# Performance work log

Measured on AMD Instinct MI355X. Metric: run time of the kernel, lower is better.

The kernel has to match this reference:

```python
import jax, jax.numpy as jnp
import numpy as np

B = 16384          # batch_size
NF = 50            # n_fields
K = 16             # embedding_dim
V = 1_000_000      # input_dim (vocab)
H = 400            # fc hidden
NNZ = B * NF


def _xavier(key, shape):
    fan_in, fan_out = shape
    lim = (6.0 / (fan_in + fan_out)) ** 0.5
    return jax.random.uniform(key, shape, minval=-lim, maxval=lim, dtype=jnp.float32)


def setup_inputs() -> dict:
    key = jax.random.key(0)
    ks = jax.random.split(key, 12)
    feats = jax.random.randint(ks[0], (NNZ,), 0, V)
    # n_fields contiguous features per sample (required by view(batch_size,-1))
    index = jnp.repeat(jnp.arange(B), NF)
    values = jax.random.uniform(ks[1], (NNZ,), dtype=jnp.float32)
    bias = jnp.zeros((1, 1), jnp.float32)
    weights = _xavier(ks[2], (V, 1))
    embedding = _xavier(ks[3], (V, K))
    d = NF * K  # 800
    W0 = _xavier(ks[4], (d, H))
    b0 = jax.random.normal(ks[5], (1, 1), jnp.float32)
    W1 = _xavier(ks[6], (H, H))
    b1 = jax.random.normal(ks[7], (1, 1), jnp.float32)
    W2 = _xavier(ks[8], (H, 1))
    b2 = jax.random.normal(ks[9], (1, 1), jnp.float32)
    return dict(index=index, feats=feats, values=values, bias=bias,
                weights=weights, embedding=embedding,
                W0=W0, b0=b0, W1=W1, b1=b1, W2=W2, b2=b2, batch_size=B)


def reference(index, feats, values, bias, weights, embedding,
              W0, b0, W1, b1, W2, b2, batch_size):
    # gather (F.embedding)
    w = weights[feats, 0]              # [nnz]
    emb = embedding[feats]             # [nnz, K]

    # first order: segment-sum of w*v, plus bias ([B] + [1,1] -> [1,B], as in torch)
    first = jax.ops.segment_sum(w * values, index, num_segments=batch_size) + bias

    # second order: FM pooling trick, fused over all K dims in one segment reduce
    ev = emb * values[:, None]                                        # [nnz, K]
    s1 = jax.ops.segment_sum(ev, index, num_segments=batch_size)      # [B, K]
    s2 = jax.ops.segment_sum(ev * ev, index, num_segments=batch_size) # [B, K]
    second = 0.5 * jnp.sum(s1 * s1 - s2, axis=1)                      # [B]

    # higher order MLP (relu on every layer, scalar biases)
    x = emb.reshape(batch_size, -1)    # [B, NF*K]
    x = jax.nn.relu(x @ W0 + b0)
    x = jax.nn.relu(x @ W1 + b1)
    x = jax.nn.relu(x @ W2 + b2)       # [B, 1]
    higher = x.reshape(-1)             # [B]

    return jax.nn.sigmoid(first + second + higher)  # [1, B]
```

## Files before the change

kernel.cpp:

```cpp
#include <hip/hip_runtime.h>
#include <hip/hip_bf16.h>


#define BATCH 16384
#define NFLD  50
#define EK    16
#define DDIM  800
#define HDIM  400
#define HPAD  416
#define NPAD  512

#define TB_W0 400
#define TB_W1 208
#define TBLK  (TB_W0 + TB_W1)
#define GBLK  (BATCH / 16)

#define MROWS 64
#define NCOLS 448
#define WCOLS 112
#define NFRAG 7
#define P1    (DDIM / 32)
#define P2    (HPAD / 32)
#define H0S   424
#define SBUF  16384
#define SBUF2 14336

#define VMCNT(N) asm volatile("s_waitcnt vmcnt(" #N ")" ::: "memory")

typedef __attribute__((ext_vector_type(8))) __bf16 bf16x8;
typedef __attribute__((ext_vector_type(4))) float  f32x4;

typedef const __attribute__((address_space(1))) unsigned int* gas_u32p;
typedef __attribute__((address_space(3))) unsigned int*       las_u32p;

__device__ __forceinline__ void gld_lds16(const void* g, void* l) {
    __builtin_amdgcn_global_load_lds((gas_u32p)g, (las_u32p)l, 16, 0, 0);
}

__device__ __forceinline__ void bar() {
    __builtin_amdgcn_sched_barrier(0);
    __builtin_amdgcn_s_barrier();
    __builtin_amdgcn_sched_barrier(0);
}

__global__ __launch_bounds__(256) void prep_kernel(
    const float* __restrict__ W0, const float* __restrict__ W1,
    __hip_bfloat16* __restrict__ W0t, __hip_bfloat16* __restrict__ W1t,
    const int* __restrict__ feats, const float* __restrict__ values,
    const float* __restrict__ biasp, const float* __restrict__ weights,
    const float* __restrict__ embedding,
    float* __restrict__ fs, __hip_bfloat16* __restrict__ x)
{
    const int bid = blockIdx.x;
    if (bid < TBLK) {
        const int which = bid >= TB_W0;
        const int i  = which ? bid - TB_W0 : bid;
        const int nx = which ? 13 : 25;
        const int bx = i % nx, by = i / nx;
        const float* src = which ? W1 : W0;
        __hip_bfloat16* dst = which ? W1t : W0t;
        const int srcK = which ? HDIM : DDIM;
        const int dstCols = which ? HPAD : DDIM;

        __shared__ float tile[32][33];
        const int tx = threadIdx.x & 31, ty = threadIdx.x >> 5;
        const int k0 = bx * 32, n0 = by * 32;
#pragma unroll
        for (int r = 0; r < 4; ++r) {
            int k = k0 + ty + r * 8;
            int n = n0 + tx;
            float v = (k < srcK && n < HDIM) ? src[(long)k * HDIM + n] : 0.f;
            tile[ty + r * 8][tx] = v;
        }
        __syncthreads();
#pragma unroll
        for (int r = 0; r < 4; ++r) {
            int n = n0 + ty + r * 8;
            int k = k0 + tx;
            if (k < dstCols)
                dst[(long)n * dstCols + k] = __float2bfloat16(tile[tx][ty + r * 8]);
        }
        return;
    }

    const int wave = threadIdx.x >> 6;
    const int lane = threadIdx.x & 63;
    const int r    = lane >> 2, c = lane & 3;
    const int sbase = (bid - TBLK) * 16 + wave * 4;

    int   f[4] = {0, 0, 0, 0};
    float v[4] = {0.f, 0.f, 0.f, 0.f};
    float wsum[4] = {0.f, 0.f, 0.f, 0.f};
#pragma unroll
    for (int q = 0; q < 4; ++q) {
        const long base = (long)(sbase + q) * NFLD;
        if (lane < NFLD) {
            f[q] = feats[base + lane];
            v[q] = values[base + lane];
            wsum[q] = weights[f[q]] * v[q];
        }
    }

    int   fj[4][4]; float vj[4][4];
#pragma unroll
    for (int q = 0; q < 4; ++q)
#pragma unroll
        for (int p = 0; p < 4; ++p) {
            const int j = p * 16 + r;
            if (p < 3 || r < 2) {
                fj[q][p] = __shfl(f[q], j);
                vj[q][p] = __shfl(v[q], j);
            }
        }
    float4 e[4][4];
#pragma unroll
    for (int q = 0; q < 4; ++q)
#pragma unroll
        for (int p = 0; p < 4; ++p)
            if (p < 3 || r < 2)
                e[q][p] = *(const float4*)(embedding + (long)fj[q][p] * EK + c * 4);

#pragma unroll
    for (int q = 0; q < 4; ++q) {
        const int s = sbase + q;
        f32x4 s1 = {0.f, 0.f, 0.f, 0.f}, s2 = {0.f, 0.f, 0.f, 0.f};
#pragma unroll
        for (int p = 0; p < 4; ++p) {
            const int j = p * 16 + r;
            if (p < 3 || r < 2) {
                f32x4 ef = {e[q][p].x, e[q][p].y, e[q][p].z, e[q][p].w};
                f32x4 ev = ef * vj[q][p];
                s1 += ev;
                s2 += ev * ev;
                __hip_bfloat16 pk[4] = {
                    __float2bfloat16(e[q][p].x), __float2bfloat16(e[q][p].y),
                    __float2bfloat16(e[q][p].z), __float2bfloat16(e[q][p].w)};
                *(uint2*)&x[(long)s * DDIM + j * EK + c * 4] = *(uint2*)pk;
            }
        }
#pragma unroll
        for (int m = 4; m <= 32; m <<= 1) {
            s1.x += __shfl_xor(s1.x, m); s1.y += __shfl_xor(s1.y, m);
            s1.z += __shfl_xor(s1.z, m); s1.w += __shfl_xor(s1.w, m);
            s2.x += __shfl_xor(s2.x, m); s2.y += __shfl_xor(s2.y, m);
            s2.z += __shfl_xor(s2.z, m); s2.w += __shfl_xor(s2.w, m);
        }
        float t = (s1.x * s1.x - s2.x) + (s1.y * s1.y - s2.y)
                + (s1.z * s1.z - s2.z) + (s1.w * s1.w - s2.w);
        t += __shfl_xor(t, 1); t += __shfl_xor(t, 2);
        float w = wsum[q];
        w += __shfl_xor(w, 1);  w += __shfl_xor(w, 2);
        w += __shfl_xor(w, 4);  w += __shfl_xor(w, 8);
        w += __shfl_xor(w, 16); w += __shfl_xor(w, 32);
        if (lane == 0) fs[s] = w + 0.5f * t + biasp[0];
    }
}

__global__ __launch_bounds__(512, 2) void fused_mlp_kernel(
    const __hip_bfloat16* __restrict__ x,
    const __hip_bfloat16* __restrict__ W0t, const __hip_bfloat16* __restrict__ W1t,
    const float* __restrict__ b0p, const float* __restrict__ b1p,
    const float* __restrict__ W2, const float* __restrict__ b2p,
    const float* __restrict__ fs, float* __restrict__ out)
{
    __shared__ __align__(16) __hip_bfloat16 sS[3 * SBUF];
    __shared__ __align__(16) __hip_bfloat16 h0p[MROWS * H0S];
    __shared__ float red[MROWS][4];

    const int tid  = threadIdx.x;
    const int wave = tid >> 6, lane = tid & 63;
    const int l16  = lane & 15, quad = lane >> 4;
    const int waveM = wave & 1, waveN = wave >> 1;
    const int m0 = blockIdx.x * MROWS;

    const int rl  = lane >> 2;
    const int swc = ((lane & 3) ^ ((lane >> 3) & 3)) * 8;
    const int qsw = (quad ^ ((l16 >> 1) & 3)) * 8;

    const float b0 = b0p[0];
    const float b1 = b1p[0];

    auto stage1 = [&](int p, int b) {
        const int k0 = p * 32;
        __hip_bfloat16* dst = sS + b * SBUF;
#pragma unroll
        for (int c = 0; c < 4; ++c) {
            const int idx = wave * 4 + c;
            const __hip_bfloat16* src = (idx < 4)
                ? x   + (long)(m0 + idx * 16 + rl) * DDIM + k0 + swc
                : W0t + (long)((idx - 4) * 16 + rl) * DDIM + k0 + swc;
            gld_lds16(src, dst + idx * 512 + lane * 8);
        }
    };

    f32x4 acc[2][NFRAG] = {};
    auto compute1 = [&](int b) {
        const __hip_bfloat16* s = sS + b * SBUF;
        bf16x8 af[2], bfr[NFRAG];
#pragma unroll
        for (int i = 0; i < 2; ++i)
            af[i] = *(const bf16x8*)&s[(waveM * 2 + i) * 512 + l16 * 32 + qsw];
#pragma unroll
        for (int j = 0; j < NFRAG; ++j)
            bfr[j] = *(const bf16x8*)&s[(4 + waveN * NFRAG + j) * 512 + l16 * 32 + qsw];
        __builtin_amdgcn_s_setprio(1);
#pragma unroll
        for (int i = 0; i < 2; ++i)
#pragma unroll
            for (int j = 0; j < NFRAG; ++j)
                acc[i][j] = __builtin_amdgcn_mfma_f32_16x16x32_bf16(
                    af[i], bfr[j], acc[i][j], 0, 0, 0);
        __builtin_amdgcn_s_setprio(0);
    };

    stage1(0, 0);
    stage1(1, 1);
    for (int p = 0; p < P1; ++p) {
        if (p + 2 < P1) stage1(p + 2, (p + 2) % 3);
        if      (p + 2 < P1) { VMCNT(8); }
        else if (p + 1 < P1) { VMCNT(4); }
        else                 { VMCNT(0); }
        bar();
        compute1(p % 3);
        bar();
    }

#pragma unroll
    for (int i = 0; i < 2; ++i)
#pragma unroll
        for (int j = 0; j < NFRAG; ++j) {
            const int col = waveN * WCOLS + j * 16 + l16;
            if (col < HPAD) {
#pragma unroll
                for (int r = 0; r < 4; ++r) {
                    const int row = waveM * 32 + i * 16 + quad * 4 + r;
                    float v = acc[i][j][r] + b0;
                    v = v > 0.f ? v : 0.f;
                    if (col >= HDIM) v = 0.f;
                    h0p[row * H0S + col] = __float2bfloat16(v);
                }
            }
        }

    auto stage2 = [&](int p, int b) {
        if (wave < 7) {
            const int k0 = p * 32;
#pragma unroll
            for (int c = 0; c < 4; ++c) {
                const int ch = wave * 4 + c;
                gld_lds16(W1t + (long)(ch * 16 + rl) * HPAD + k0 + swc,
                          sS + b * SBUF2 + ch * 512 + lane * 8);
            }
        }
    };

    f32x4 acc2[2][NFRAG] = {};
    float w2v[NFRAG];
#pragma unroll
    for (int j = 0; j < NFRAG; ++j) {
        const int col = waveN * WCOLS + j * 16 + l16;
        w2v[j] = (col < HDIM) ? W2[col] : 0.f;
    }
    auto compute2 = [&](int p, int b) {
        const __hip_bfloat16* s = sS + b * SBUF2;
        bf16x8 af[2], bfr[NFRAG];
#pragma unroll
        for (int i = 0; i < 2; ++i)
            af[i] = *(const bf16x8*)&h0p[(waveM * 32 + i * 16 + l16) * H0S + p * 32 + quad * 8];
#pragma unroll
        for (int j = 0; j < NFRAG; ++j)
            bfr[j] = *(const bf16x8*)&s[(waveN * NFRAG + j) * 512 + l16 * 32 + qsw];
        __builtin_amdgcn_s_setprio(1);
#pragma unroll
        for (int i = 0; i < 2; ++i)
#pragma unroll
            for (int j = 0; j < NFRAG; ++j)
                acc2[i][j] = __builtin_amdgcn_mfma_f32_16x16x32_bf16(
                    af[i], bfr[j], acc2[i][j], 0, 0, 0);
        __builtin_amdgcn_s_setprio(0);
    };

    stage2(0, 0);
    stage2(1, 1);
    asm volatile("s_waitcnt lgkmcnt(0)" ::: "memory");
    bar();

    for (int p = 0; p < P2; ++p) {
        if (p + 2 < P2) stage2(p + 2, (p + 2) % 3);
        if      (p + 2 < P2) { VMCNT(8); }
        else if (p + 1 < P2) { VMCNT(4); }
        else                 { VMCNT(0); }
        bar();
        compute2(p, p % 3);
        bar();
    }

#pragma unroll
    for (int i = 0; i < 2; ++i)
#pragma unroll
        for (int r = 0; r < 4; ++r) {
            float ps = 0.f;
#pragma unroll
            for (int j = 0; j < NFRAG; ++j) {
                float v = acc2[i][j][r] + b1;
                v = v > 0.f ? v : 0.f;
                ps += v * w2v[j];
            }
            ps += __shfl_xor(ps, 1); ps += __shfl_xor(ps, 2);
            ps += __shfl_xor(ps, 4); ps += __shfl_xor(ps, 8);
            if (l16 == 0)
                red[waveM * 32 + i * 16 + quad * 4 + r][waveN] = ps;
        }
    __syncthreads();

    if (tid < MROWS) {
        const float s = (red[tid][0] + red[tid][1]) + (red[tid][2] + red[tid][3]);
        float hv = s + b2p[0];
        hv = hv > 0.f ? hv : 0.f;
        const float z = fs[m0 + tid] + hv;
        out[m0 + tid] = 1.f / (1.f + __expf(-z));
    }
}

extern "C" void kernel_launch(void* const* d_in, const int* in_sizes, int n_in,
                              void* d_out, int out_size, void* d_ws, size_t ws_size,
                              hipStream_t stream)
{
    const int*   feats     = (const int*)d_in[1];
    const float* values    = (const float*)d_in[2];
    const float* bias      = (const float*)d_in[3];
    const float* weights   = (const float*)d_in[4];
    const float* embedding = (const float*)d_in[5];
    const float* W0 = (const float*)d_in[6];
    const float* b0 = (const float*)d_in[7];
    const float* W1 = (const float*)d_in[8];
    const float* b1 = (const float*)d_in[9];
    const float* W2 = (const float*)d_in[10];
    const float* b2 = (const float*)d_in[11];

    char* ws = (char*)d_ws;
    size_t off = 0;
    auto alloc = [&](size_t bytes) {
        void* p = ws + off;
        off += (bytes + 255) & ~(size_t)255;
        return p;
    };
    float*          fs   = (float*)alloc((size_t)BATCH * 4);
    __hip_bfloat16* x    = (__hip_bfloat16*)alloc((size_t)BATCH * DDIM * 2);
    __hip_bfloat16* W0t  = (__hip_bfloat16*)alloc((size_t)NPAD * DDIM * 2);
    __hip_bfloat16* W1t  = (__hip_bfloat16*)alloc((size_t)NPAD * HPAD * 2);
    (void)ws_size; (void)in_sizes; (void)n_in; (void)out_size;

    prep_kernel<<<dim3(TBLK + GBLK), 256, 0, stream>>>(
        W0, W1, W0t, W1t, feats, values, bias, weights, embedding, fs, x);
    fused_mlp_kernel<<<dim3(BATCH / MROWS), 512, 0, stream>>>(
        x, W0t, W1t, b0, b1, W2, b2, fs, (float*)d_out);
}
```

Before: 178.1 us.

## Use one barrier per K-step and prefetch W1 tiles during layer-0 epilogue

The two triple-buffered GEMM loops now wait for the current stage and hit a single barrier before issuing the next prefetch, replacing the two barriers per iteration. The first two W1 tiles are issued before the h0 bias/ReLU write-out, so that load overlaps the epilogue. LDS is merged into one raw byte buffer with explicit offsets, and the reduction buffer is read as a float4. Dropping the trailing barrier depends on the buffer being prefetched into always having been consumed in an earlier iteration, which triple buffering is meant to ensure.

```diff
diff --git a/kernel.cpp b/kernel.cpp
--- a/kernel.cpp
+++ b/kernel.cpp
@@ -22,8 +22,12 @@
 #define P1    (DDIM / 32)
 #define P2    (HPAD / 32)
 #define H0S   424
-#define SBUF  16384
-#define SBUF2 14336
+
+#define PH1B(b) ((b) * 32768)
+#define PH2B(b) ((b) * 28672)
+#define H0OFF   98304
+#define REDOFF  152576
+#define LDSSZ   153600
 
 #define VMCNT(N) asm volatile("s_waitcnt vmcnt(" #N ")" ::: "memory")
 
@@ -163,9 +167,9 @@
     const float* __restrict__ W2, const float* __restrict__ b2p,
     const float* __restrict__ fs, float* __restrict__ out)
 {
-    __shared__ __align__(16) __hip_bfloat16 sS[3 * SBUF];
-    __shared__ __align__(16) __hip_bfloat16 h0p[MROWS * H0S];
-    __shared__ float red[MROWS][4];
+    __shared__ __align__(16) char lds[LDSSZ];
+    __hip_bfloat16* h0p = (__hip_bfloat16*)(lds + H0OFF);
+    float*          red = (float*)(lds + REDOFF);
 
     const int tid  = threadIdx.x;
     const int wave = tid >> 6, lane = tid & 63;
@@ -182,20 +186,20 @@
 
     auto stage1 = [&](int p, int b) {
         const int k0 = p * 32;
-        __hip_bfloat16* dst = sS + b * SBUF;
+        char* dst = lds + PH1B(b);
 #pragma unroll
         for (int c = 0; c < 4; ++c) {
             const int idx = wave * 4 + c;
             const __hip_bfloat16* src = (idx < 4)
                 ? x   + (long)(m0 + idx * 16 + rl) * DDIM + k0 + swc
                 : W0t + (long)((idx - 4) * 16 + rl) * DDIM + k0 + swc;
-            gld_lds16(src, dst + idx * 512 + lane * 8);
+            gld_lds16(src, dst + idx * 1024 + lane * 16);
         }
     };
 
     f32x4 acc[2][NFRAG] = {};
     auto compute1 = [&](int b) {
-        const __hip_bfloat16* s = sS + b * SBUF;
+        const __hip_bfloat16* s = (const __hip_bfloat16*)(lds + PH1B(b));
         bf16x8 af[2], bfr[NFRAG];
 #pragma unroll
         for (int i = 0; i < 2; ++i)
@@ -216,14 +220,26 @@
     stage1(0, 0);
     stage1(1, 1);
     for (int p = 0; p < P1; ++p) {
+        if (p + 1 < P1) { VMCNT(4); } else { VMCNT(0); }
+        bar();
         if (p + 2 < P1) stage1(p + 2, (p + 2) % 3);
-        if      (p + 2 < P1) { VMCNT(8); }
-        else if (p + 1 < P1) { VMCNT(4); }
-        else                 { VMCNT(0); }
-        bar();
         compute1(p % 3);
-        bar();
-    }
+    }
+    bar();
+
+    auto stage2 = [&](int p, int b) {
+        if (wave < 7) {
+            const int k0 = p * 32;
+#pragma unroll
+            for (int c = 0; c < 4; ++c) {
+                const int ch = wave * 4 + c;
+                gld_lds16(W1t + (long)(ch * 16 + rl) * HPAD + k0 + swc,
+                          lds + PH2B(b) + ch * 1024 + lane * 16);
+            }
+        }
+    };
+    stage2(0, 0);
+    stage2(1, 1);
 
 #pragma unroll
     for (int i = 0; i < 2; ++i)
@@ -242,18 +258,6 @@
             }
         }
 
-    auto stage2 = [&](int p, int b) {
-        if (wave < 7) {
-            const int k0 = p * 32;
-#pragma unroll
-            for (int c = 0; c < 4; ++c) {
-                const int ch = wave * 4 + c;
-                gld_lds16(W1t + (long)(ch * 16 + rl) * HPAD + k0 + swc,
-                          sS + b * SBUF2 + ch * 512 + lane * 8);
-            }
-        }
-    };
-
     f32x4 acc2[2][NFRAG] = {};
     float w2v[NFRAG];
 #pragma unroll
@@ -262,7 +266,7 @@
         w2v[j] = (col < HDIM) ? W2[col] : 0.f;
     }
     auto compute2 = [&](int p, int b) {
-        const __hip_bfloat16* s = sS + b * SBUF2;
+        const __hip_bfloat16* s = (const __hip_bfloat16*)(lds + PH2B(b));
         bf16x8 af[2], bfr[NFRAG];
 #pragma unroll
         for (int i = 0; i < 2; ++i)
@@ -280,19 +284,14 @@
         __builtin_amdgcn_s_setprio(0);
     };
 
-    stage2(0, 0);
-    stage2(1, 1);
     asm volatile("s_waitcnt lgkmcnt(0)" ::: "memory");
     bar();
 
     for (int p = 0; p < P2; ++p) {
+        if (p + 1 < P2) { VMCNT(4); } else { VMCNT(0); }
+        bar();
         if (p + 2 < P2) stage2(p + 2, (p + 2) % 3);
-        if      (p + 2 < P2) { VMCNT(8); }
-        else if (p + 1 < P2) { VMCNT(4); }
-        else                 { VMCNT(0); }
-        bar();
         compute2(p, p % 3);
-        bar();
     }
 
 #pragma unroll
@@ -309,12 +308,13 @@
             ps += __shfl_xor(ps, 1); ps += __shfl_xor(ps, 2);
             ps += __shfl_xor(ps, 4); ps += __shfl_xor(ps, 8);
             if (l16 == 0)
-                red[waveM * 32 + i * 16 + quad * 4 + r][waveN] = ps;
+                red[(waveM * 32 + i * 16 + quad * 4 + r) * 4 + waveN] = ps;
         }
     __syncthreads();
 
     if (tid < MROWS) {
-        const float s = (red[tid][0] + red[tid][1]) + (red[tid][2] + red[tid][3]);
+        const float4 rr = *(const float4*)&red[tid * 4];
+        const float s = (rr.x + rr.y) + (rr.z + rr.w);
         float hv = s + b2p[0];
         hv = hv > 0.f ? hv : 0.f;
         const float z = fs[m0 + tid] + hv;
```

Measured after the change: 165.9 us, median of 2. 6.8% less time.
